# Kernel optimization log

Hardware: AMD Instinct MI355X
Metric: run time of the kernel (lower is better)

Reference implementation:

```python
import jax, jax.numpy as jnp
import numpy as np
import math

N_EXPERTS = 32
K_SEL = 4
IN_C = 1024
OUT_C = 1024
BATCH = 4096


def setup_inputs() -> dict:
    key = jax.random.key(0)
    kx, ki, kw = jax.random.split(key, 3)
    x = jax.random.normal(kx, (BATCH, IN_C), dtype=jnp.float32)
    idx = jax.random.randint(ki, (BATCH, K_SEL), 0, N_EXPERTS, dtype=jnp.int64)
    # xavier_uniform with gain=sqrt(2) (relu) on (n, in_c, out_c):
    # fan_in = in_c, fan_out = out_c for each expert's 2D slice
    gain = math.sqrt(2.0)
    bound = gain * math.sqrt(6.0 / (IN_C + OUT_C))
    w = jax.random.uniform(kw, (N_EXPERTS, IN_C, OUT_C), dtype=jnp.float32,
                           minval=-bound, maxval=bound)
    b = jnp.zeros((N_EXPERTS, 1, OUT_C), dtype=jnp.float32)
    return {"x": x, "idx": idx, "w": w, "b": b}


def reference(x, idx, w, b):
    # Per-sample selection of k of n FC layers:
    # out[bat, k, o] = relu( x[bat] @ w[idx[bat,k]] + b[idx[bat,k]] )
    # Computed densely over all n experts then gathered, which avoids
    # materializing a (B, K, in_c, out_c) gathered-weight tensor.
    y_all = jnp.einsum('bi,nio->bno', x, w) + b[:, 0, :][None]  # (B, n, out_c)
    out = jnp.take_along_axis(y_all, idx[:, :, None], axis=1)   # (B, K, out_c)
    return jax.nn.relu(out)
```

## Files before the change

kernel.cpp:

```cpp
#include <hip/hip_runtime.h>
#include <hip/hip_bf16.h>

#define N_EXPERTS 32
#define K_SEL 4
#define IN_C 1024
#define OUT_C 1024
#define BATCH 4096
#define NTOK (BATCH * K_SEL)

#define BM 128
#define BN 128
#define BK 64
#define MAX_TILES (N_EXPERTS + NTOK / BM)

#define XB_ELEMS (BATCH * IN_C)
#define CTRL_OFF_BYTES ((size_t)XB_ELEMS * 2)

#define WS_NTILES 0
#define WS_TABLE 8
#define WS_ROWLIST (WS_TABLE + MAX_TILES * 4)
#define CTRL_INTS (WS_ROWLIST + NTOK)
#define WS_COUNTS (CTRL_INTS)
#define WS_CURSOR (CTRL_INTS + 32)

typedef __attribute__((ext_vector_type(4))) float f32x4;
typedef __attribute__((ext_vector_type(8))) short bf16x8;
typedef __attribute__((ext_vector_type(8))) unsigned short u16x8;

__device__ __forceinline__ unsigned short f2bf(float f) {
    union { float f; unsigned u; } v; v.f = f;
    unsigned r = v.u + 0x7fffu + ((v.u >> 16) & 1u);
    return (unsigned short)(r >> 16);
}

__device__ __forceinline__ void gload16(const void* g, void* l) {
    __builtin_amdgcn_global_load_lds(
        (const __attribute__((address_space(1))) unsigned int*)g,
        (__attribute__((address_space(3))) unsigned int*)l, 16, 0, 0);
}


#define XCONV_B0 1
#define XCONV_NB (XB_ELEMS / 2048)
#define PREP_NWG (XCONV_B0 + XCONV_NB)

__global__ __launch_bounds__(256)
void prep_kernel(const float* __restrict__ x, const int* __restrict__ idx,
                 unsigned short* __restrict__ xb, int* __restrict__ ctrl) {
    const int bid = blockIdx.x;
    const int t = threadIdx.x;

    if (bid >= XCONV_B0) {
        int i = ((bid - XCONV_B0) * 256 + t) << 3;
        f32x4 v0 = *(const f32x4*)(x + i);
        f32x4 v1 = *(const f32x4*)(x + i + 4);
        u16x8 o;
        o[0] = f2bf(v0[0]); o[1] = f2bf(v0[1]); o[2] = f2bf(v0[2]); o[3] = f2bf(v0[3]);
        o[4] = f2bf(v1[0]); o[5] = f2bf(v1[1]); o[6] = f2bf(v1[2]); o[7] = f2bf(v1[3]);
        *(u16x8*)(xb + i) = o;
    } else {
        __shared__ int cnt[N_EXPERTS], base[N_EXPERTS], tbase[N_EXPERTS];
        if (t < N_EXPERTS) cnt[t] = 0;
        __syncthreads();
        #pragma unroll 4
        for (int i = 0; i < NTOK / 256; ++i) {
            int e = idx[i * 256 + t] & (N_EXPERTS - 1);
            atomicAdd(&cnt[e], 1);
        }
        __syncthreads();
        if (t == 0) {
            int off = 0, tiles = 0;
            for (int e = 0; e < N_EXPERTS; ++e) {
                base[e] = off;
                tbase[e] = tiles;
                int c = cnt[e];
                tiles += (c + BM - 1) / BM;
                off += c;
            }
            ctrl[WS_NTILES] = tiles;
        }
        __syncthreads();
        if (t < N_EXPERTS) {
            int c = cnt[t], off = base[t], tt = tbase[t];
            for (int u = 0; u < c; u += BM, ++tt) {
                ctrl[WS_TABLE + tt * 4 + 0] = t;
                ctrl[WS_TABLE + tt * 4 + 1] = off + u;
                ctrl[WS_TABLE + tt * 4 + 2] = (c - u) < BM ? (c - u) : BM;
            }
            cnt[t] = off;
        }
        __syncthreads();
        #pragma unroll 4
        for (int i = 0; i < NTOK / 256; ++i) {
            int s = i * 256 + t;
            int e = idx[s] & (N_EXPERTS - 1);
            int p = atomicAdd(&cnt[e], 1);
            ctrl[WS_ROWLIST + p] = s;
        }
    }
}


__global__ __launch_bounds__(256, 3)
void gemm_kernel(const unsigned short* __restrict__ xb,
                 const float* __restrict__ w,
                 const float* __restrict__ bias,
                 const int* __restrict__ ctrl,
                 float* __restrict__ out) {
    const int swz = ((int)blockIdx.x & 7) * ((MAX_TILES * 8) >> 3) + ((int)blockIdx.x >> 3);
    const int tileIdx = swz >> 3;
    const int ntiles = ctrl[WS_NTILES];
    if (tileIdx >= ntiles) return;
    const int e     = ctrl[WS_TABLE + tileIdx * 4 + 0];
    const int list0 = ctrl[WS_TABLE + tileIdx * 4 + 1];
    const int nrows = ctrl[WS_TABLE + tileIdx * 4 + 2];
    const int n0 = (swz & 7) * BN;

    __shared__ unsigned short As[BM][BK];
    __shared__ unsigned short Bs[BN][BK];
    __shared__ int rowtok[BM];

    const int t = threadIdx.x;
    const int lane = t & 63, wv = t >> 6;

    if (t < BM) {
        int r = t < nrows ? t : nrows - 1;
        rowtok[t] = ctrl[WS_ROWLIST + list0 + r];
    }
    __syncthreads();

    const int cg = (lane & 7) ^ (lane >> 3);
    const unsigned short* asrc[4];
    #pragma unroll
    for (int i = 0; i < 4; ++i) {
        int row = (wv << 5) + (i << 3) + (lane >> 3);
        asrc[i] = xb + (size_t)(rowtok[row] >> 2) * IN_C + (cg << 3);
    }

    const int q = t & 31, o = t >> 5;
    const float* bbase = w + ((size_t)e << 20) + (size_t)(o << 3 << 10) + n0 + (q << 2);

    const int wr = (t >> 7) & 1;
    const int wc = (t >> 6) & 1;
    const int lrow = lane & 15, lq = lane >> 4;
    const int afo0 = ((lq) ^ (lrow & 7)) << 4;
    const int afo1 = ((4 + lq) ^ (lrow & 7)) << 4;
    const char* aB = (const char*)&As[wr * 64 + lrow][0];
    const char* bB = (const char*)&Bs[wc * 64 + lrow][0];
    int bfo[2][4];
    #pragma unroll
    for (int kk = 0; kk < 2; ++kk)
        #pragma unroll
        for (int nf = 0; nf < 4; ++nf)
            bfo[kk][nf] = ((((kk << 2) + lq) ^ (lrow & 7) ^ ((2 * nf + (lrow >> 3)) & 7)) << 4);

    f32x4 acc[4][4];
    #pragma unroll
    for (int m = 0; m < 4; ++m)
        #pragma unroll
        for (int n = 0; n < 4; ++n) acc[m][n] = (f32x4)0.f;

    f32x4 breg[8];
    #pragma unroll
    for (int r = 0; r < 8; ++r)
        breg[r] = *(const f32x4*)(bbase + ((size_t)r << 10));

    for (int k0 = 0; k0 < IN_C; k0 += BK) {
        asm volatile("s_waitcnt lgkmcnt(0)" ::: "memory");
        __builtin_amdgcn_s_barrier();
        #pragma unroll
        for (int i = 0; i < 4; ++i)
            gload16(asrc[i] + k0, &As[(wv << 5) + (i << 3)][0]);
        __builtin_amdgcn_sched_barrier(0);
        #pragma unroll
        for (int j = 0; j < 4; ++j) {
            const int n = (q << 2) + j;
            const int phys = o ^ (n & 7) ^ ((n >> 3) & 7);
            u16x8 ov;
            #pragma unroll
            for (int r = 0; r < 8; ++r) ov[r] = f2bf(breg[r][j]);
            *(u16x8*)&Bs[n][phys << 3] = ov;
        }
        __builtin_amdgcn_sched_barrier(0);
        {
            const int kn = (k0 + BK < IN_C) ? (k0 + BK) : 0;
            const float* bs2 = bbase + ((size_t)kn << 10);
            #pragma unroll
            for (int r = 0; r < 8; ++r)
                breg[r] = *(const f32x4*)(bs2 + ((size_t)r << 10));
        }
        __builtin_amdgcn_sched_barrier(0);
        asm volatile("s_waitcnt vmcnt(8)" ::: "memory");
        asm volatile("s_waitcnt lgkmcnt(0)" ::: "memory");
        __builtin_amdgcn_sched_barrier(0);
        __builtin_amdgcn_s_barrier();
        #pragma unroll
        for (int kk = 0; kk < 2; ++kk) {
            const int afo = kk ? afo1 : afo0;
            bf16x8 a[4], b[4];
            #pragma unroll
            for (int m = 0; m < 4; ++m) a[m] = *(const bf16x8*)(aB + m * 2048 + afo);
            #pragma unroll
            for (int n = 0; n < 4; ++n) b[n] = *(const bf16x8*)(bB + n * 2048 + bfo[kk][n]);
            #pragma unroll
            for (int m = 0; m < 4; ++m)
                #pragma unroll
                for (int n = 0; n < 4; ++n)
                    acc[m][n] = __builtin_amdgcn_mfma_f32_16x16x32_bf16(a[m], b[n], acc[m][n], 0, 0, 0);
        }
    }

    #pragma unroll
    for (int m = 0; m < 4; ++m) {
        #pragma unroll
        for (int j = 0; j < 4; ++j) {
            int row = wr * 64 + m * 16 + lq * 4 + j;
            if (row < nrows) {
                int s = rowtok[row];
                float* orow = out + (size_t)s * OUT_C;
                #pragma unroll
                for (int n = 0; n < 4; ++n) {
                    int col = n0 + wc * 64 + n * 16 + lrow;
                    float vv = acc[m][n][j] + bias[e * OUT_C + col];
                    orow[col] = vv > 0.f ? vv : 0.f;
                }
            }
        }
    }
}


__global__ void count_kernel(const int* __restrict__ idx, int* __restrict__ ctrl) {
    int s = blockIdx.x * blockDim.x + threadIdx.x;
    if (s < NTOK) atomicAdd(&ctrl[WS_COUNTS + (idx[s] & (N_EXPERTS - 1))], 1);
}

__global__ void scan_kernel(int* __restrict__ ctrl) {
    if (threadIdx.x != 0) return;
    int off = 0, tiles = 0;
    for (int e = 0; e < N_EXPERTS; ++e) {
        int c = ctrl[WS_COUNTS + e];
        ctrl[WS_CURSOR + e] = off;
        for (int t = 0; t < c; t += BM) {
            ctrl[WS_TABLE + tiles * 4 + 0] = e;
            ctrl[WS_TABLE + tiles * 4 + 1] = off + t;
            ctrl[WS_TABLE + tiles * 4 + 2] = (c - t) < BM ? (c - t) : BM;
            ++tiles;
        }
        off += c;
    }
    ctrl[WS_NTILES] = tiles;
}

__global__ void scatter_kernel(const int* __restrict__ idx, int* __restrict__ ctrl) {
    int s = blockIdx.x * blockDim.x + threadIdx.x;
    if (s < NTOK) {
        int e = idx[s] & (N_EXPERTS - 1);
        int p = atomicAdd(&ctrl[WS_CURSOR + e], 1);
        ctrl[WS_ROWLIST + p] = s;
    }
}

__global__ __launch_bounds__(256, 2)
void gemm_f32_kernel(const float* __restrict__ x, const float* __restrict__ w,
                     const float* __restrict__ bias, const int* __restrict__ ctrl,
                     float* __restrict__ out) {
    int ntiles = ctrl[WS_NTILES];
    if ((int)blockIdx.x >= ntiles) return;
    const int e     = ctrl[WS_TABLE + blockIdx.x * 4 + 0];
    const int list0 = ctrl[WS_TABLE + blockIdx.x * 4 + 1];
    const int nrows = ctrl[WS_TABLE + blockIdx.x * 4 + 2];
    const int n0 = blockIdx.y * BN;

    __shared__ unsigned short As2[BM][40];
    __shared__ unsigned short Bs2[BN][40];
    __shared__ int rowtok[BM];

    const int t = threadIdx.x;
    if (t < BM) {
        int r = t < nrows ? t : nrows - 1;
        rowtok[t] = ctrl[WS_ROWLIST + list0 + r];
    }
    __syncthreads();

    const int arow = t >> 1, acol0 = (t & 1) * 16;
    const int brow = t >> 3, bcol0 = (t & 7) * 16;
    const float* xbase = x + (size_t)(rowtok[arow] >> 2) * IN_C + acol0;
    const float* wbase = w + (size_t)e * IN_C * OUT_C + (size_t)brow * OUT_C + n0 + bcol0;

    const int lane = t & 63, wid = t >> 6;
    const int wr = wid >> 1, wc = wid & 1;
    const int lrow = lane & 15, lq = lane >> 4;

    f32x4 acc[4][4];
    #pragma unroll
    for (int m = 0; m < 4; ++m)
        #pragma unroll
        for (int n = 0; n < 4; ++n) acc[m][n] = (f32x4)0.f;

    for (int k0 = 0; k0 < IN_C; k0 += 32) {
        __syncthreads();
        #pragma unroll
        for (int u = 0; u < 4; ++u) {
            f32x4 v = *(const f32x4*)(xbase + k0 + 4 * u);
            ushort4 pk;
            pk.x = f2bf(v[0]); pk.y = f2bf(v[1]); pk.z = f2bf(v[2]); pk.w = f2bf(v[3]);
            *(ushort4*)&As2[arow][acol0 + 4 * u] = pk;
        }
        #pragma unroll
        for (int u = 0; u < 4; ++u) {
            f32x4 v = *(const f32x4*)(wbase + (size_t)k0 * OUT_C + 4 * u);
            Bs2[bcol0 + 4 * u + 0][brow] = f2bf(v[0]);
            Bs2[bcol0 + 4 * u + 1][brow] = f2bf(v[1]);
            Bs2[bcol0 + 4 * u + 2][brow] = f2bf(v[2]);
            Bs2[bcol0 + 4 * u + 3][brow] = f2bf(v[3]);
        }
        __syncthreads();

        bf16x8 a[4], b[4];
        #pragma unroll
        for (int m = 0; m < 4; ++m) a[m] = *(const bf16x8*)&As2[wr * 64 + m * 16 + lrow][lq * 8];
        #pragma unroll
        for (int n = 0; n < 4; ++n) b[n] = *(const bf16x8*)&Bs2[wc * 64 + n * 16 + lrow][lq * 8];
        #pragma unroll
        for (int m = 0; m < 4; ++m)
            #pragma unroll
            for (int n = 0; n < 4; ++n)
                acc[m][n] = __builtin_amdgcn_mfma_f32_16x16x32_bf16(a[m], b[n], acc[m][n], 0, 0, 0);
    }

    #pragma unroll
    for (int m = 0; m < 4; ++m) {
        #pragma unroll
        for (int j = 0; j < 4; ++j) {
            int row = wr * 64 + m * 16 + lq * 4 + j;
            if (row < nrows) {
                int s = rowtok[row];
                float* orow = out + (size_t)s * OUT_C;
                #pragma unroll
                for (int n = 0; n < 4; ++n) {
                    int col = n0 + wc * 64 + n * 16 + lrow;
                    float vv = acc[m][n][j] + bias[e * OUT_C + col];
                    orow[col] = vv > 0.f ? vv : 0.f;
                }
            }
        }
    }
}


extern "C" void kernel_launch(void* const* d_in, const int* in_sizes, int n_in,
                              void* d_out, int out_size, void* d_ws, size_t ws_size,
                              hipStream_t stream) {
    const float* x    = (const float*)d_in[0];
    const int*   idx  = (const int*)d_in[1];
    const float* w    = (const float*)d_in[2];
    const float* bias = (const float*)d_in[3];
    float* out = (float*)d_out;

    const size_t need = CTRL_OFF_BYTES + (size_t)(CTRL_INTS + 64) * sizeof(int);
    if (ws_size >= need) {
        unsigned short* xb = (unsigned short*)d_ws;
        int* ctrl = (int*)((char*)d_ws + CTRL_OFF_BYTES);

        prep_kernel<<<PREP_NWG, 256, 0, stream>>>(x, idx, xb, ctrl);
        gemm_kernel<<<MAX_TILES * 8, 256, 0, stream>>>(xb, w, bias, ctrl, out);
    } else {
        int* ctrl = (int*)d_ws;
        hipMemsetAsync(ctrl, 0, (CTRL_INTS + 64) * sizeof(int), stream);
        count_kernel<<<NTOK / 256, 256, 0, stream>>>(idx, ctrl);
        scan_kernel<<<1, 64, 0, stream>>>(ctrl);
        scatter_kernel<<<NTOK / 256, 256, 0, stream>>>(idx, ctrl);
        dim3 grid(MAX_TILES, OUT_C / BN);
        gemm_f32_kernel<<<grid, 256, 0, stream>>>(x, w, bias, ctrl, out);
    }
}
```

Measured before the change: 104.8 us.

## Double expert tile rows to 256 so each block reuses weights more

Grows the per-expert token tile from 128 to 256 rows. Each wave now covers 64 rows by the full 128 output columns, with 4x8 accumulators. This halves how often each expert's fp32 weight slice is loaded and converted to bf16, which targets weight bandwidth and conversion cost. In exchange it raises register pressure, lowers occupancy to 2 blocks per CU, and gives coarser load balance with fewer tiles. It also skips the redundant last-iteration prefetch.

New measurement: 110.7 us. 5.6% more time.

```diff
diff --git a/kernel.cpp b/kernel.cpp
--- a/kernel.cpp
+++ b/kernel.cpp
@@ -9,9 +9,12 @@
 #define NTOK (BATCH * K_SEL)
 
 #define BM 128
+#define BM2 256
 #define BN 128
 #define BK 64
+#define NKT (IN_C / BK)
 #define MAX_TILES (N_EXPERTS + NTOK / BM)
+#define MAX_T2 (N_EXPERTS + NTOK / BM2)
 
 #define XB_ELEMS (BATCH * IN_C)
 #define CTRL_OFF_BYTES ((size_t)XB_ELEMS * 2)
@@ -74,7 +77,7 @@
                 base[e] = off;
                 tbase[e] = tiles;
                 int c = cnt[e];
-                tiles += (c + BM - 1) / BM;
+                tiles += (c + BM2 - 1) / BM2;
                 off += c;
             }
             ctrl[WS_NTILES] = tiles;
@@ -82,10 +85,10 @@
         __syncthreads();
         if (t < N_EXPERTS) {
             int c = cnt[t], off = base[t], tt = tbase[t];
-            for (int u = 0; u < c; u += BM, ++tt) {
+            for (int u = 0; u < c; u += BM2, ++tt) {
                 ctrl[WS_TABLE + tt * 4 + 0] = t;
                 ctrl[WS_TABLE + tt * 4 + 1] = off + u;
-                ctrl[WS_TABLE + tt * 4 + 2] = (c - u) < BM ? (c - u) : BM;
+                ctrl[WS_TABLE + tt * 4 + 2] = (c - u) < BM2 ? (c - u) : BM2;
             }
             cnt[t] = off;
         }
@@ -101,13 +104,14 @@
 }
 
 
-__global__ __launch_bounds__(256, 3)
+__global__ __launch_bounds__(256, 2)
 void gemm_kernel(const unsigned short* __restrict__ xb,
                  const float* __restrict__ w,
                  const float* __restrict__ bias,
                  const int* __restrict__ ctrl,
                  float* __restrict__ out) {
-    const int swz = ((int)blockIdx.x & 7) * ((MAX_TILES * 8) >> 3) + ((int)blockIdx.x >> 3);
+    const int bid = (int)blockIdx.x;
+    const int swz = (bid & 7) * MAX_T2 + (bid >> 3);
     const int tileIdx = swz >> 3;
     const int ntiles = ctrl[WS_NTILES];
     if (tileIdx >= ntiles) return;
@@ -116,49 +120,54 @@
     const int nrows = ctrl[WS_TABLE + tileIdx * 4 + 2];
     const int n0 = (swz & 7) * BN;
 
-    __shared__ unsigned short As[BM][BK];
+    __shared__ unsigned short As[BM2][BK];
     __shared__ unsigned short Bs[BN][BK];
-    __shared__ int rowtok[BM];
+    __shared__ int rowtok[BM2];
 
     const int t = threadIdx.x;
     const int lane = t & 63, wv = t >> 6;
 
-    if (t < BM) {
-        int r = t < nrows ? t : nrows - 1;
-        rowtok[t] = ctrl[WS_ROWLIST + list0 + r];
+    {
+        int r0 = t < nrows ? t : nrows - 1;
+        rowtok[t] = ctrl[WS_ROWLIST + list0 + r0];
+        int r1 = (t + 256) < nrows ? (t + 256) : nrows - 1;
+        if (t + 256 < BM2) {}
+        r1 = (t + 0);
+    }
+    {
+        int ra = t < nrows ? t : nrows - 1;
+        rowtok[t] = ctrl[WS_ROWLIST + list0 + ra];
     }
     __syncthreads();
 
     const int cg = (lane & 7) ^ (lane >> 3);
-    const unsigned short* asrc[4];
-    #pragma unroll
-    for (int i = 0; i < 4; ++i) {
-        int row = (wv << 5) + (i << 3) + (lane >> 3);
+    const unsigned short* asrc[8];
+    #pragma unroll
+    for (int i = 0; i < 8; ++i) {
+        int row = (wv << 6) + (i << 3) + (lane >> 3);
         asrc[i] = xb + (size_t)(rowtok[row] >> 2) * IN_C + (cg << 3);
     }
 
     const int q = t & 31, o = t >> 5;
-    const float* bbase = w + ((size_t)e << 20) + (size_t)(o << 3 << 10) + n0 + (q << 2);
-
-    const int wr = (t >> 7) & 1;
-    const int wc = (t >> 6) & 1;
+    const float* bbase = w + ((size_t)e << 20) + ((size_t)(o << 3) << 10) + n0 + (q << 2);
+
     const int lrow = lane & 15, lq = lane >> 4;
     const int afo0 = ((lq) ^ (lrow & 7)) << 4;
     const int afo1 = ((4 + lq) ^ (lrow & 7)) << 4;
-    const char* aB = (const char*)&As[wr * 64 + lrow][0];
-    const char* bB = (const char*)&Bs[wc * 64 + lrow][0];
-    int bfo[2][4];
+    const char* aB = (const char*)&As[(wv << 6) + lrow][0];
+    const char* bB = (const char*)&Bs[lrow][0];
+    int bfo[2][8];
     #pragma unroll
     for (int kk = 0; kk < 2; ++kk)
         #pragma unroll
-        for (int nf = 0; nf < 4; ++nf)
+        for (int nf = 0; nf < 8; ++nf)
             bfo[kk][nf] = ((((kk << 2) + lq) ^ (lrow & 7) ^ ((2 * nf + (lrow >> 3)) & 7)) << 4);
 
-    f32x4 acc[4][4];
+    f32x4 acc[4][8];
     #pragma unroll
     for (int m = 0; m < 4; ++m)
         #pragma unroll
-        for (int n = 0; n < 4; ++n) acc[m][n] = (f32x4)0.f;
+        for (int n = 0; n < 8; ++n) acc[m][n] = (f32x4)0.f;
 
     f32x4 breg[8];
     #pragma unroll
@@ -169,8 +178,8 @@
         asm volatile("s_waitcnt lgkmcnt(0)" ::: "memory");
         __builtin_amdgcn_s_barrier();
         #pragma unroll
-        for (int i = 0; i < 4; ++i)
-            gload16(asrc[i] + k0, &As[(wv << 5) + (i << 3)][0]);
+        for (int i = 0; i < 8; ++i)
+            gload16(asrc[i] + k0, &As[(wv << 6) + (i << 3)][0]);
         __builtin_amdgcn_sched_barrier(0);
         #pragma unroll
         for (int j = 0; j < 4; ++j) {
@@ -182,32 +191,152 @@
             *(u16x8*)&Bs[n][phys << 3] = ov;
         }
         __builtin_amdgcn_sched_barrier(0);
-        {
-            const int kn = (k0 + BK < IN_C) ? (k0 + BK) : 0;
-            const float* bs2 = bbase + ((size_t)kn << 10);
+        if (k0 + BK < IN_C) {
+            const float* bs2 = bbase + ((size_t)(k0 + BK) << 10);
             #pragma unroll
             for (int r = 0; r < 8; ++r)
                 breg[r] = *(const f32x4*)(bs2 + ((size_t)r << 10));
-        }
-        __builtin_amdgcn_sched_barrier(0);
-        asm volatile("s_waitcnt vmcnt(8)" ::: "memory");
+            __builtin_amdgcn_sched_barrier(0);
+            asm volatile("s_waitcnt vmcnt(8)" ::: "memory");
+        } else {
+            asm volatile("s_waitcnt vmcnt(0)" ::: "memory");
+        }
         asm volatile("s_waitcnt lgkmcnt(0)" ::: "memory");
         __builtin_amdgcn_sched_barrier(0);
         __builtin_amdgcn_s_barrier();
         #pragma unroll
         for (int kk = 0; kk < 2; ++kk) {
             const int afo = kk ? afo1 : afo0;
-            bf16x8 a[4], b[4];
+            bf16x8 a[4], b[8];
             #pragma unroll
             for (int m = 0; m < 4; ++m) a[m] = *(const bf16x8*)(aB + m * 2048 + afo);
             #pragma unroll
-            for (int n = 0; n < 4; ++n) b[n] = *(const bf16x8*)(bB + n * 2048 + bfo[kk][n]);
+            for (int n = 0; n < 8; ++n) b[n] = *(const bf16x8*)(bB + n * 2048 + bfo[kk][n]);
             #pragma unroll
             for (int m = 0; m < 4; ++m)
                 #pragma unroll
-                for (int n = 0; n < 4; ++n)
+                for (int n = 0; n < 8; ++n)
                     acc[m][n] = __builtin_amdgcn_mfma_f32_16x16x32_bf16(a[m], b[n], acc[m][n], 0, 0, 0);
         }
+    }
+
+    #pragma unroll
+    for (int m = 0; m < 4; ++m) {
+        #pragma unroll
+        for (int j = 0; j < 4; ++j) {
+            int row = (wv << 6) + m * 16 + lq * 4 + j;
+            if (row < nrows) {
+                int s = rowtok[row];
+                float* orow = out + (size_t)s * OUT_C;
+                #pragma unroll
+                for (int n = 0; n < 8; ++n) {
+                    int col = n0 + n * 16 + lrow;
+                    float vv = acc[m][n][j] + bias[e * OUT_C + col];
+                    orow[col] = vv > 0.f ? vv : 0.f;
+                }
+            }
+        }
+    }
+}
+
+
+__global__ void count_kernel(const int* __restrict__ idx, int* __restrict__ ctrl) {
+    int s = blockIdx.x * blockDim.x + threadIdx.x;
+    if (s < NTOK) atomicAdd(&ctrl[WS_COUNTS + (idx[s] & (N_EXPERTS - 1))], 1);
+}
+
+__global__ void scan_kernel(int* __restrict__ ctrl) {
+    if (threadIdx.x != 0) return;
+    int off = 0, tiles = 0;
+    for (int e = 0; e < N_EXPERTS; ++e) {
+        int c = ctrl[WS_COUNTS + e];
+        ctrl[WS_CURSOR + e] = off;
+        for (int t = 0; t < c; t += BM) {
+            ctrl[WS_TABLE + tiles * 4 + 0] = e;
+            ctrl[WS_TABLE + tiles * 4 + 1] = off + t;
+            ctrl[WS_TABLE + tiles * 4 + 2] = (c - t) < BM ? (c - t) : BM;
+            ++tiles;
+        }
+        off += c;
+    }
+    ctrl[WS_NTILES] = tiles;
+}
+
+__global__ void scatter_kernel(const int* __restrict__ idx, int* __restrict__ ctrl) {
+    int s = blockIdx.x * blockDim.x + threadIdx.x;
+    if (s < NTOK) {
+        int e = idx[s] & (N_EXPERTS - 1);
+        int p = atomicAdd(&ctrl[WS_CURSOR + e], 1);
+        ctrl[WS_ROWLIST + p] = s;
+    }
+}
+
+__global__ __launch_bounds__(256, 2)
+void gemm_f32_kernel(const float* __restrict__ x, const float* __restrict__ w,
+                     const float* __restrict__ bias, const int* __restrict__ ctrl,
+                     float* __restrict__ out) {
+    int ntiles = ctrl[WS_NTILES];
+    if ((int)blockIdx.x >= ntiles) return;
+    const int e     = ctrl[WS_TABLE + blockIdx.x * 4 + 0];
+    const int list0 = ctrl[WS_TABLE + blockIdx.x * 4 + 1];
+    const int nrows = ctrl[WS_TABLE + blockIdx.x * 4 + 2];
+    const int n0 = blockIdx.y * BN;
+
+    __shared__ unsigned short As2[BM][40];
+    __shared__ unsigned short Bs2[BN][40];
+    __shared__ int rowtok[BM];
+
+    const int t = threadIdx.x;
+    if (t < BM) {
+        int r = t < nrows ? t : nrows - 1;
+        rowtok[t] = ctrl[WS_ROWLIST + list0 + r];
+    }
+    __syncthreads();
+
+    const int arow = t >> 1, acol0 = (t & 1) * 16;
+    const int brow = t >> 3, bcol0 = (t & 7) * 16;
+    const float* xbase = x + (size_t)(rowtok[arow] >> 2) * IN_C + acol0;
+    const float* wbase = w + (size_t)e * IN_C * OUT_C + (size_t)brow * OUT_C + n0 + bcol0;
+
+    const int lane = t & 63, wid = t >> 6;
+    const int wr = wid >> 1, wc = wid & 1;
+    const int lrow = lane & 15, lq = lane >> 4;
+
+    f32x4 acc[4][4];
+    #pragma unroll
+    for (int m = 0; m < 4; ++m)
+        #pragma unroll
+        for (int n = 0; n < 4; ++n) acc[m][n] = (f32x4)0.f;
+
+    for (int k0 = 0; k0 < IN_C; k0 += 32) {
+        __syncthreads();
+        #pragma unroll
+        for (int u = 0; u < 4; ++u) {
+            f32x4 v = *(const f32x4*)(xbase + k0 + 4 * u);
+            ushort4 pk;
+            pk.x = f2bf(v[0]); pk.y = f2bf(v[1]); pk.z = f2bf(v[2]); pk.w = f2bf(v[3]);
+            *(ushort4*)&As2[arow][acol0 + 4 * u] = pk;
+        }
+        #pragma unroll
+        for (int u = 0; u < 4; ++u) {
+            f32x4 v = *(const f32x4*)(wbase + (size_t)k0 * OUT_C + 4 * u);
+            Bs2[bcol0 + 4 * u + 0][brow] = f2bf(v[0]);
+            Bs2[bcol0 + 4 * u + 1][brow] = f2bf(v[1]);
+            Bs2[bcol0 + 4 * u + 2][brow] = f2bf(v[2]);
+            Bs2[bcol0 + 4 * u + 3][brow] = f2bf(v[3]);
+        }
+        __syncthreads();
+
+        bf16x8 a[4], b[4];
+        #pragma unroll
+        for (int m = 0; m < 4; ++m) a[m] = *(const bf16x8*)&As2[wr * 64 + m * 16 + lrow][lq * 8];
+        #pragma unroll
+        for (int n = 0; n < 4; ++n) b[n] = *(const bf16x8*)&Bs2[wc * 64 + n * 16 + lrow][lq * 8];
+        #pragma unroll
+        for (int m = 0; m < 4; ++m)
+            #pragma unroll
+            for (int n = 0; n < 4; ++n)
+                acc[m][n] = __builtin_amdgcn_mfma_f32_16x16x32_bf16(a[m], b[n], acc[m][n], 0, 0, 0);
     }
 
     #pragma unroll
@@ -230,125 +359,6 @@
 }
 
 
-__global__ void count_kernel(const int* __restrict__ idx, int* __restrict__ ctrl) {
-    int s = blockIdx.x * blockDim.x + threadIdx.x;
-    if (s < NTOK) atomicAdd(&ctrl[WS_COUNTS + (idx[s] & (N_EXPERTS - 1))], 1);
-}
-
-__global__ void scan_kernel(int* __restrict__ ctrl) {
-    if (threadIdx.x != 0) return;
-    int off = 0, tiles = 0;
-    for (int e = 0; e < N_EXPERTS; ++e) {
-        int c = ctrl[WS_COUNTS + e];
-        ctrl[WS_CURSOR + e] = off;
-        for (int t = 0; t < c; t += BM) {
-            ctrl[WS_TABLE + tiles * 4 + 0] = e;
-            ctrl[WS_TABLE + tiles * 4 + 1] = off + t;
-            ctrl[WS_TABLE + tiles * 4 + 2] = (c - t) < BM ? (c - t) : BM;
-            ++tiles;
-        }
-        off += c;
-    }
-    ctrl[WS_NTILES] = tiles;
-}
-
-__global__ void scatter_kernel(const int* __restrict__ idx, int* __restrict__ ctrl) {
-    int s = blockIdx.x * blockDim.x + threadIdx.x;
-    if (s < NTOK) {
-        int e = idx[s] & (N_EXPERTS - 1);
-        int p = atomicAdd(&ctrl[WS_CURSOR + e], 1);
-        ctrl[WS_ROWLIST + p] = s;
-    }
-}
-
-__global__ __launch_bounds__(256, 2)
-void gemm_f32_kernel(const float* __restrict__ x, const float* __restrict__ w,
-                     const float* __restrict__ bias, const int* __restrict__ ctrl,
-                     float* __restrict__ out) {
-    int ntiles = ctrl[WS_NTILES];
-    if ((int)blockIdx.x >= ntiles) return;
-    const int e     = ctrl[WS_TABLE + blockIdx.x * 4 + 0];
-    const int list0 = ctrl[WS_TABLE + blockIdx.x * 4 + 1];
-    const int nrows = ctrl[WS_TABLE + blockIdx.x * 4 + 2];
-    const int n0 = blockIdx.y * BN;
-
-    __shared__ unsigned short As2[BM][40];
-    __shared__ unsigned short Bs2[BN][40];
-    __shared__ int rowtok[BM];
-
-    const int t = threadIdx.x;
-    if (t < BM) {
-        int r = t < nrows ? t : nrows - 1;
-        rowtok[t] = ctrl[WS_ROWLIST + list0 + r];
-    }
-    __syncthreads();
-
-    const int arow = t >> 1, acol0 = (t & 1) * 16;
-    const int brow = t >> 3, bcol0 = (t & 7) * 16;
-    const float* xbase = x + (size_t)(rowtok[arow] >> 2) * IN_C + acol0;
-    const float* wbase = w + (size_t)e * IN_C * OUT_C + (size_t)brow * OUT_C + n0 + bcol0;
-
-    const int lane = t & 63, wid = t >> 6;
-    const int wr = wid >> 1, wc = wid & 1;
-    const int lrow = lane & 15, lq = lane >> 4;
-
-    f32x4 acc[4][4];
-    #pragma unroll
-    for (int m = 0; m < 4; ++m)
-        #pragma unroll
-        for (int n = 0; n < 4; ++n) acc[m][n] = (f32x4)0.f;
-
-    for (int k0 = 0; k0 < IN_C; k0 += 32) {
-        __syncthreads();
-        #pragma unroll
-        for (int u = 0; u < 4; ++u) {
-            f32x4 v = *(const f32x4*)(xbase + k0 + 4 * u);
-            ushort4 pk;
-            pk.x = f2bf(v[0]); pk.y = f2bf(v[1]); pk.z = f2bf(v[2]); pk.w = f2bf(v[3]);
-            *(ushort4*)&As2[arow][acol0 + 4 * u] = pk;
-        }
-        #pragma unroll
-        for (int u = 0; u < 4; ++u) {
-            f32x4 v = *(const f32x4*)(wbase + (size_t)k0 * OUT_C + 4 * u);
-            Bs2[bcol0 + 4 * u + 0][brow] = f2bf(v[0]);
-            Bs2[bcol0 + 4 * u + 1][brow] = f2bf(v[1]);
-            Bs2[bcol0 + 4 * u + 2][brow] = f2bf(v[2]);
-            Bs2[bcol0 + 4 * u + 3][brow] = f2bf(v[3]);
-        }
-        __syncthreads();
-
-        bf16x8 a[4], b[4];
-        #pragma unroll
-        for (int m = 0; m < 4; ++m) a[m] = *(const bf16x8*)&As2[wr * 64 + m * 16 + lrow][lq * 8];
-        #pragma unroll
-        for (int n = 0; n < 4; ++n) b[n] = *(const bf16x8*)&Bs2[wc * 64 + n * 16 + lrow][lq * 8];
-        #pragma unroll
-        for (int m = 0; m < 4; ++m)
-            #pragma unroll
-            for (int n = 0; n < 4; ++n)
-                acc[m][n] = __builtin_amdgcn_mfma_f32_16x16x32_bf16(a[m], b[n], acc[m][n], 0, 0, 0);
-    }
-
-    #pragma unroll
-    for (int m = 0; m < 4; ++m) {
-        #pragma unroll
-        for (int j = 0; j < 4; ++j) {
-            int row = wr * 64 + m * 16 + lq * 4 + j;
-            if (row < nrows) {
-                int s = rowtok[row];
-                float* orow = out + (size_t)s * OUT_C;
-                #pragma unroll
-                for (int n = 0; n < 4; ++n) {
-                    int col = n0 + wc * 64 + n * 16 + lrow;
-                    float vv = acc[m][n][j] + bias[e * OUT_C + col];
-                    orow[col] = vv > 0.f ? vv : 0.f;
-                }
-            }
-        }
-    }
-}
-
-
 extern "C" void kernel_launch(void* const* d_in, const int* in_sizes, int n_in,
                               void* d_out, int out_size, void* d_ws, size_t ws_size,
                               hipStream_t stream) {
@@ -364,7 +374,7 @@
         int* ctrl = (int*)((char*)d_ws + CTRL_OFF_BYTES);
 
         prep_kernel<<<PREP_NWG, 256, 0, stream>>>(x, idx, xb, ctrl);
-        gemm_kernel<<<MAX_TILES * 8, 256, 0, stream>>>(xb, w, bias, ctrl, out);
+        gemm_kernel<<<MAX_T2 * 8, 256, 0, stream>>>(xb, w, bias, ctrl, out);
     } else {
         int* ctrl = (int*)d_ws;
         hipMemsetAsync(ctrl, 0, (CTRL_INTS + 64) * sizeof(int), stream);
```

## Cooperatively pre-convert expert weights to bf16 once per chunk inside GEMM

Applied to the files above, without the earlier changes.

Workgroups sharing an expert/column block claim 64-row chunks of the fp32 weight slice through atomic flags. Each claimed chunk is converted to bf16 once into a workspace buffer, and each group spin-waits until all 16 chunks for its slice are done. The main loop then streams bf16 weights instead of fp32, which halves B traffic per tile and removes redundant conversions across the M-tiles of the same expert. The cost is an extra memset, a 64MB bf16 write, and spin-wait synchronization that could stall or deadlock if the claiming groups are not resident.

Result: slower. 372.5 us (+255.5%).

```diff
diff --git a/kernel.cpp b/kernel.cpp
--- a/kernel.cpp
+++ b/kernel.cpp
@@ -14,7 +14,11 @@
 #define MAX_TILES (N_EXPERTS + NTOK / BM)
 
 #define XB_ELEMS (BATCH * IN_C)
+#define WT_ELEMS (N_EXPERTS * IN_C * OUT_C)
 #define CTRL_OFF_BYTES ((size_t)XB_ELEMS * 2)
+#define WT_OFF_BYTES (CTRL_OFF_BYTES + 131072)
+#define FLAGS_OFF_BYTES (WT_OFF_BYTES + (size_t)WT_ELEMS * 2)
+#define N_CHUNKS (N_EXPERTS * 8 * 16)
 
 #define WS_NTILES 0
 #define WS_TABLE 8
@@ -26,6 +30,7 @@
 typedef __attribute__((ext_vector_type(4))) float f32x4;
 typedef __attribute__((ext_vector_type(8))) short bf16x8;
 typedef __attribute__((ext_vector_type(8))) unsigned short u16x8;
+typedef __attribute__((ext_vector_type(4))) unsigned short u16x4;
 
 __device__ __forceinline__ unsigned short f2bf(float f) {
     union { float f; unsigned u; } v; v.f = f;
@@ -104,8 +109,10 @@
 __global__ __launch_bounds__(256, 3)
 void gemm_kernel(const unsigned short* __restrict__ xb,
                  const float* __restrict__ w,
+                 unsigned short* __restrict__ wt,
                  const float* __restrict__ bias,
                  const int* __restrict__ ctrl,
+                 int* claim, int* done,
                  float* __restrict__ out) {
     const int swz = ((int)blockIdx.x & 7) * ((MAX_TILES * 8) >> 3) + ((int)blockIdx.x >> 3);
     const int tileIdx = swz >> 3;
@@ -114,11 +121,13 @@
     const int e     = ctrl[WS_TABLE + tileIdx * 4 + 0];
     const int list0 = ctrl[WS_TABLE + tileIdx * 4 + 1];
     const int nrows = ctrl[WS_TABLE + tileIdx * 4 + 2];
-    const int n0 = (swz & 7) * BN;
+    const int nb = swz & 7;
+    const int n0 = nb * BN;
 
     __shared__ unsigned short As[BM][BK];
     __shared__ unsigned short Bs[BN][BK];
     __shared__ int rowtok[BM];
+    __shared__ int got;
 
     const int t = threadIdx.x;
     const int lane = t & 63, wv = t >> 6;
@@ -127,18 +136,50 @@
         int r = t < nrows ? t : nrows - 1;
         rowtok[t] = ctrl[WS_ROWLIST + list0 + r];
     }
+
+    const int cbase = (e * 8 + nb) * 16;
+    const float* psrc = w + ((size_t)e << 20) + n0;
+    unsigned short* pdst = wt + ((size_t)e << 20) + n0;
+    for (int c = 0; c < 16; ++c) {
+        __syncthreads();
+        if (t == 0) got = (atomicCAS(&claim[cbase + c], 0, 1) == 0);
+        __syncthreads();
+        if (got) {
+            const size_t rowoff = (size_t)(c << 6) << 10;
+            #pragma unroll
+            for (int u = 0; u < 4; ++u) {
+                int un = (u << 8) + t;
+                int r = un >> 4, cg = (un & 15) << 3;
+                f32x4 v0 = *(const f32x4*)(psrc + rowoff + ((size_t)r << 10) + cg);
+                f32x4 v1 = *(const f32x4*)(psrc + rowoff + ((size_t)r << 10) + cg + 4);
+                u16x8 ov;
+                ov[0] = f2bf(v0[0]); ov[1] = f2bf(v0[1]); ov[2] = f2bf(v0[2]); ov[3] = f2bf(v0[3]);
+                ov[4] = f2bf(v1[0]); ov[5] = f2bf(v1[1]); ov[6] = f2bf(v1[2]); ov[7] = f2bf(v1[3]);
+                *(u16x8*)(pdst + rowoff + ((size_t)r << 10) + cg) = ov;
+            }
+            __syncthreads();
+            if (t == 0)
+                __hip_atomic_store(&done[cbase + c], 1, __ATOMIC_RELEASE, __HIP_MEMORY_SCOPE_AGENT);
+        }
+    }
+    if (t == 0) {
+        #pragma unroll 1
+        for (int c = 0; c < 16; ++c)
+            while (__hip_atomic_load(&done[cbase + c], __ATOMIC_RELAXED, __HIP_MEMORY_SCOPE_AGENT) == 0)
+                __builtin_amdgcn_s_sleep(2);
+        __builtin_amdgcn_fence(__ATOMIC_ACQUIRE, "agent");
+    }
     __syncthreads();
 
-    const int cg = (lane & 7) ^ (lane >> 3);
+    const int cg2 = (lane & 7) ^ (lane >> 3);
     const unsigned short* asrc[4];
     #pragma unroll
     for (int i = 0; i < 4; ++i) {
         int row = (wv << 5) + (i << 3) + (lane >> 3);
-        asrc[i] = xb + (size_t)(rowtok[row] >> 2) * IN_C + (cg << 3);
-    }
-
+        asrc[i] = xb + (size_t)(rowtok[row] >> 2) * IN_C + (cg2 << 3);
+    }
     const int q = t & 31, o = t >> 5;
-    const float* bbase = w + ((size_t)e << 20) + (size_t)(o << 3 << 10) + n0 + (q << 2);
+    const unsigned short* bbase = wt + ((size_t)e << 20) + ((size_t)(o << 3) << 10) + n0 + (q << 2);
 
     const int wr = (t >> 7) & 1;
     const int wc = (t >> 6) & 1;
@@ -160,10 +201,10 @@
         #pragma unroll
         for (int n = 0; n < 4; ++n) acc[m][n] = (f32x4)0.f;
 
-    f32x4 breg[8];
+    u16x4 breg[8];
     #pragma unroll
     for (int r = 0; r < 8; ++r)
-        breg[r] = *(const f32x4*)(bbase + ((size_t)r << 10));
+        breg[r] = *(const u16x4*)(bbase + ((size_t)r << 10));
 
     for (int k0 = 0; k0 < IN_C; k0 += BK) {
         asm volatile("s_waitcnt lgkmcnt(0)" ::: "memory");
@@ -178,19 +219,20 @@
             const int phys = o ^ (n & 7) ^ ((n >> 3) & 7);
             u16x8 ov;
             #pragma unroll
-            for (int r = 0; r < 8; ++r) ov[r] = f2bf(breg[r][j]);
+            for (int r = 0; r < 8; ++r) ov[r] = breg[r][j];
             *(u16x8*)&Bs[n][phys << 3] = ov;
         }
         __builtin_amdgcn_sched_barrier(0);
-        {
-            const int kn = (k0 + BK < IN_C) ? (k0 + BK) : 0;
-            const float* bs2 = bbase + ((size_t)kn << 10);
+        if (k0 + BK < IN_C) {
+            const unsigned short* bs2 = bbase + ((size_t)(k0 + BK) << 10);
             #pragma unroll
             for (int r = 0; r < 8; ++r)
-                breg[r] = *(const f32x4*)(bs2 + ((size_t)r << 10));
-        }
-        __builtin_amdgcn_sched_barrier(0);
-        asm volatile("s_waitcnt vmcnt(8)" ::: "memory");
+                breg[r] = *(const u16x4*)(bs2 + ((size_t)r << 10));
+            __builtin_amdgcn_sched_barrier(0);
+            asm volatile("s_waitcnt vmcnt(8)" ::: "memory");
+        } else {
+            asm volatile("s_waitcnt vmcnt(0)" ::: "memory");
+        }
         asm volatile("s_waitcnt lgkmcnt(0)" ::: "memory");
         __builtin_amdgcn_sched_barrier(0);
         __builtin_amdgcn_s_barrier();
@@ -358,13 +400,17 @@
     const float* bias = (const float*)d_in[3];
     float* out = (float*)d_out;
 
-    const size_t need = CTRL_OFF_BYTES + (size_t)(CTRL_INTS + 64) * sizeof(int);
+    const size_t need = FLAGS_OFF_BYTES + (size_t)N_CHUNKS * 2 * sizeof(int);
     if (ws_size >= need) {
         unsigned short* xb = (unsigned short*)d_ws;
         int* ctrl = (int*)((char*)d_ws + CTRL_OFF_BYTES);
-
+        unsigned short* wt = (unsigned short*)((char*)d_ws + WT_OFF_BYTES);
+        int* claim = (int*)((char*)d_ws + FLAGS_OFF_BYTES);
+        int* done = claim + N_CHUNKS;
+
+        hipMemsetAsync(claim, 0, (size_t)N_CHUNKS * 2 * sizeof(int), stream);
         prep_kernel<<<PREP_NWG, 256, 0, stream>>>(x, idx, xb, ctrl);
-        gemm_kernel<<<MAX_TILES * 8, 256, 0, stream>>>(xb, w, bias, ctrl, out);
+        gemm_kernel<<<MAX_TILES * 8, 256, 0, stream>>>(xb, w, wt, bias, ctrl, claim, done, out);
     } else {
         int* ctrl = (int*)d_ws;
         hipMemsetAsync(ctrl, 0, (CTRL_INTS + 64) * sizeof(int), stream);
```
